# Optimization experiments

Measured on AMD Instinct MI355X. Metric: run time of the kernel, lower is better.

Reference implementation:

```python
import jax, jax.numpy as jnp
import numpy as np

N = 8192      # number of tree nodes
H = 256       # lstm_hiddens
D = 300       # word_dims (in_dim)
V = 50000     # vocab (n_embed)
K = 4         # max children per node (4-ary tree)
OUT = 4       # category_num


def _make_tree():
    # Static 4-ary tree: node i's children are 4i+1..4i+4 (if < N).
    idx = np.arange(N)[:, None] * K + 1 + np.arange(K)[None, :]
    mask = (idx < N).astype(np.float32)
    idx = np.where(idx < N, idx, 0)
    return jnp.asarray(idx, dtype=jnp.int32), jnp.asarray(mask, dtype=jnp.float32)


def setup_inputs() -> dict:
    key = jax.random.key(0)
    ks = jax.random.split(key, 6)
    xs = jax.random.randint(ks[0], (N,), 0, V, dtype=jnp.int32)
    emb_table = jax.random.normal(ks[1], (V, D), jnp.float32) * 0.1
    Wx = jax.random.normal(ks[2], (4, H, D), jnp.float32) * (1.0 / np.sqrt(D))
    bx = jnp.zeros((4, H), jnp.float32)
    Wh = jax.random.normal(ks[3], (4, H, H), jnp.float32) * (1.0 / np.sqrt(H))
    bh = jnp.zeros((4, H), jnp.float32)
    Wout = jax.random.normal(ks[4], (OUT, H), jnp.float32) * (1.0 / np.sqrt(H))
    bout = jnp.zeros((OUT,), jnp.float32)
    child_idx, child_mask = _make_tree()
    return dict(xs=xs, child_idx=child_idx, child_mask=child_mask,
                emb_table=emb_table, Wx=Wx, bx=bx, Wh=Wh, bh=bh,
                Wout=Wout, bout=bout)


def reference(xs, child_idx, child_mask, emb_table, Wx, bx, Wh, bh, Wout, bout):
    # Embedding lookup (dropout is identity in eval)
    X = emb_table[xs]                                   # [N, D]
    # Precompute all x-side gate projections in one batched matmul.
    # Gate order: 0=i, 1=f, 2=o, 3=u  (matches ix/fx/ox/ux).
    gx = jnp.einsum('ghd,nd->ngh', Wx, X) + bx          # [N, 4, H]

    Wh_i, Wh_f, Wh_o, Wh_u = Wh[0], Wh[1], Wh[2], Wh[3]
    bh_i, bh_f, bh_o, bh_u = bh[0], bh[1], bh[2], bh[3]

    def step(carry, i):
        Hbuf, Cbuf = carry
        cidx = child_idx[i]                              # [K]
        m = child_mask[i][:, None]                       # [K, 1]
        Hc = Hbuf[cidx] * m                              # [K, H] masked child h
        Cc = Cbuf[cidx] * m                              # [K, H] masked child c
        hs = Hc.sum(0)                                   # child_h_sum
        g = gx[i]                                        # [4, H]
        ig = jax.nn.sigmoid(g[0] + Wh_i @ hs + bh_i)
        og = jax.nn.sigmoid(g[2] + Wh_o @ hs + bh_o)
        ug = jnp.tanh(g[3] + Wh_u @ hs + bh_u)
        f = jax.nn.sigmoid(g[1] + Hc @ Wh_f.T + bh_f)    # [K, H] per-child forget
        c = ig * ug + (f * Cc).sum(0)                    # masked children have Cc=0
        h = og * jnp.tanh(c)
        return (Hbuf.at[i].set(h), Cbuf.at[i].set(c)), None

    order = jnp.arange(N - 1, -1, -1)                    # children before parents
    init = (jnp.zeros((N, H), X.dtype), jnp.zeros((N, H), X.dtype))
    (Hbuf, _), _ = jax.lax.scan(step, init, order)

    logits = Wout @ Hbuf[0] + bout                       # root output
    return jax.nn.log_softmax(logits)
```

## Files before the change

### kernel.cpp

```cpp
#include <hip/hip_runtime.h>


#define N_NODES 8192
#define HDIM 256
#define DDIM 300
#define GXC 1024
#define LEAF_FIRST 2048
#define WH_STRIDE 65536
#define XI(k) ((k) + (((k) >> 6) << 2))

__device__ __forceinline__ float sigf(float x) { return 1.0f / (1.0f + __expf(-x)); }

__global__ __launch_bounds__(256) void gx_gemm(
    const int* __restrict__ xs, const float* __restrict__ emb,
    const float* __restrict__ Wx, const float* __restrict__ bx,
    float* __restrict__ gx)
{
    const int lid  = blockIdx.x + blockIdx.y * gridDim.x;
    const int rowt = (lid & 7) * 8 + ((lid >> 3) & 7);
    const int colt = lid >> 6;
    const int n0 = rowt * 128;
    const int c0 = colt * 128;
    if (n0 >= LEAF_FIRST && (colt == 2 || colt == 3)) return;

    __shared__ __align__(16) float As[16][132];
    __shared__ __align__(16) float Bs[16][132];
    const int tid  = threadIdx.x;
    const int sr   = tid >> 1;
    const int sk8  = (tid & 1) << 3;
    const int trow = (tid >> 4) << 3;
    const int tcol = (tid & 15) << 3;

    const long arow = (long)xs[n0 + sr] * DDIM;
    const long brow = (long)(c0 + sr) * DDIM;

    float acc[8][8] = {};

    float4 a0 = *(const float4*)(emb + arow + sk8);
    float4 a1 = *(const float4*)(emb + arow + sk8 + 4);
    float4 b0 = *(const float4*)(Wx  + brow + sk8);
    float4 b1 = *(const float4*)(Wx  + brow + sk8 + 4);

    for (int k0 = 0; k0 < DDIM; k0 += 16) {
        __syncthreads();
        As[sk8+0][sr] = a0.x; As[sk8+1][sr] = a0.y; As[sk8+2][sr] = a0.z; As[sk8+3][sr] = a0.w;
        As[sk8+4][sr] = a1.x; As[sk8+5][sr] = a1.y; As[sk8+6][sr] = a1.z; As[sk8+7][sr] = a1.w;
        Bs[sk8+0][sr] = b0.x; Bs[sk8+1][sr] = b0.y; Bs[sk8+2][sr] = b0.z; Bs[sk8+3][sr] = b0.w;
        Bs[sk8+4][sr] = b1.x; Bs[sk8+5][sr] = b1.y; Bs[sk8+6][sr] = b1.z; Bs[sk8+7][sr] = b1.w;
        __syncthreads();

        const int kn = k0 + 16;
        a0 = make_float4(0.f,0.f,0.f,0.f); a1 = a0; b0 = a0; b1 = a0;
        if (kn < DDIM) {
            if (kn + sk8 < DDIM) {
                a0 = *(const float4*)(emb + arow + kn + sk8);
                b0 = *(const float4*)(Wx  + brow + kn + sk8);
            }
            if (kn + sk8 + 4 < DDIM) {
                a1 = *(const float4*)(emb + arow + kn + sk8 + 4);
                b1 = *(const float4*)(Wx  + brow + kn + sk8 + 4);
            }
        }

        #pragma unroll
        for (int k = 0; k < 16; k++) {
            const float4 av0 = *(const float4*)&As[k][trow];
            const float4 av1 = *(const float4*)&As[k][trow + 4];
            const float4 bv0 = *(const float4*)&Bs[k][tcol];
            const float4 bv1 = *(const float4*)&Bs[k][tcol + 4];
            const float aa[8] = {av0.x,av0.y,av0.z,av0.w,av1.x,av1.y,av1.z,av1.w};
            const float bb[8] = {bv0.x,bv0.y,bv0.z,bv0.w,bv1.x,bv1.y,bv1.z,bv1.w};
            #pragma unroll
            for (int i = 0; i < 8; i++)
                #pragma unroll
                for (int j = 0; j < 8; j++)
                    acc[i][j] = fmaf(aa[i], bb[j], acc[i][j]);
        }
    }

    const int col = c0 + tcol;
    const float4 bxa = *(const float4*)(bx + col);
    const float4 bxb = *(const float4*)(bx + col + 4);
    #pragma unroll
    for (int i = 0; i < 8; i++) {
        float4 r0, r1;
        r0.x = acc[i][0] + bxa.x; r0.y = acc[i][1] + bxa.y;
        r0.z = acc[i][2] + bxa.z; r0.w = acc[i][3] + bxa.w;
        r1.x = acc[i][4] + bxb.x; r1.y = acc[i][5] + bxb.y;
        r1.z = acc[i][6] + bxb.z; r1.w = acc[i][7] + bxb.w;
        float* dst = gx + (long)(n0 + trow + i) * GXC + col;
        *(float4*)dst = r0;
        *(float4*)(dst + 4) = r1;
    }
}

__global__ __launch_bounds__(256) void leaf_kernel(
    const float* __restrict__ gx, const float* __restrict__ bh,
    float* __restrict__ Hb, float* __restrict__ Cb)
{
    const int t = threadIdx.x;
    const float bi = bh[t], bo = bh[512 + t], bu = bh[768 + t];
    #pragma unroll
    for (int s = 0; s < 4; s++) {
        const int node = LEAF_FIRST + blockIdx.x * 4 + s;
        const float* g = gx + (long)node * GXC;
        const float gi = g[t]       + bi;
        const float go = g[512 + t] + bo;
        const float gu = g[768 + t] + bu;
        const float c  = sigf(gi) * tanhf(gu);
        const float h  = sigf(go) * tanhf(c);
        Hb[(long)node * HDIM + t] = h;
        Cb[(long)node * HDIM + t] = c;
    }
}

__global__ __launch_bounds__(256) void level_gemm(
    int first, int M, const float* __restrict__ Hb,
    const int* __restrict__ child_idx, const float* __restrict__ child_mask,
    const float* __restrict__ Wh, float* __restrict__ D)
{
    __shared__ __align__(16) float Xs[16][68];
    __shared__ __align__(16) float Ws[16][68];
    const int tid  = threadIdx.x;
    const int sec  = blockIdx.y;
    const int c0   = blockIdx.x * 64;
    const int r0   = blockIdx.z * 64;
    const int sr   = tid >> 2;
    const int sk   = (tid & 3) << 2;
    const int trow = (tid >> 4) << 2;
    const int tcol = (tid & 15) << 2;

    const float* Wg;
    if      (sec == 0) Wg = Wh;
    else if (sec == 1) Wg = Wh + 2 * WH_STRIDE;
    else if (sec == 2) Wg = Wh + 3 * WH_STRIDE;
    else               Wg = Wh + 1 * WH_STRIDE;

    const int  nl    = c0 + sr;
    const bool valid = nl < M;
    int   ci[4];
    float cm[4] = {0.f, 0.f, 0.f, 0.f};
    if (valid) {
        const int n = first + nl;
        if (sec < 3) {
            #pragma unroll
            for (int k = 0; k < 4; k++) {
                ci[k] = child_idx[n * 4 + k];
                cm[k] = child_mask[n * 4 + k];
            }
        } else {
            ci[0] = child_idx[n * 4 + (sec - 3)];
            cm[0] = child_mask[n * 4 + (sec - 3)];
        }
    }
    const long wrow = (long)(r0 + sr) * HDIM;

    float acc[4][4] = {};
    float4 hvr[4], wvr;

    #pragma unroll
    for (int k = 0; k < 4; k++) hvr[k] = make_float4(0.f, 0.f, 0.f, 0.f);
    if (valid) {
        if (sec < 3) {
            #pragma unroll
            for (int k = 0; k < 4; k++)
                if (cm[k] != 0.f)
                    hvr[k] = *(const float4*)(Hb + ci[k] * HDIM + sk);
        } else if (cm[0] != 0.f) {
            hvr[0] = *(const float4*)(Hb + ci[0] * HDIM + sk);
        }
    }
    wvr = *(const float4*)(Wg + wrow + sk);

    for (int k0 = 0; k0 < HDIM; k0 += 16) {
        __syncthreads();
        float4 xv;
        xv.x = hvr[0].x + hvr[1].x + hvr[2].x + hvr[3].x;
        xv.y = hvr[0].y + hvr[1].y + hvr[2].y + hvr[3].y;
        xv.z = hvr[0].z + hvr[1].z + hvr[2].z + hvr[3].z;
        xv.w = hvr[0].w + hvr[1].w + hvr[2].w + hvr[3].w;
        Xs[sk+0][sr] = xv.x; Xs[sk+1][sr] = xv.y; Xs[sk+2][sr] = xv.z; Xs[sk+3][sr] = xv.w;
        Ws[sk+0][sr] = wvr.x; Ws[sk+1][sr] = wvr.y; Ws[sk+2][sr] = wvr.z; Ws[sk+3][sr] = wvr.w;
        __syncthreads();

        const int kn = k0 + 16;
        if (kn < HDIM) {
            #pragma unroll
            for (int k = 0; k < 4; k++) hvr[k] = make_float4(0.f, 0.f, 0.f, 0.f);
            if (valid) {
                if (sec < 3) {
                    #pragma unroll
                    for (int k = 0; k < 4; k++)
                        if (cm[k] != 0.f)
                            hvr[k] = *(const float4*)(Hb + ci[k] * HDIM + kn + sk);
                } else if (cm[0] != 0.f) {
                    hvr[0] = *(const float4*)(Hb + ci[0] * HDIM + kn + sk);
                }
            }
            wvr = *(const float4*)(Wg + wrow + kn + sk);
        }

        #pragma unroll
        for (int k = 0; k < 16; k++) {
            float4 a = *(const float4*)&Ws[k][trow];
            float4 b = *(const float4*)&Xs[k][tcol];
            float avv[4] = {a.x, a.y, a.z, a.w};
            float bvv[4] = {b.x, b.y, b.z, b.w};
            #pragma unroll
            for (int i = 0; i < 4; i++)
                #pragma unroll
                for (int j = 0; j < 4; j++)
                    acc[i][j] = fmaf(avv[i], bvv[j], acc[i][j]);
        }
    }

    #pragma unroll
    for (int j = 0; j < 4; j++) {
        const int col = c0 + tcol + j;
        if (col < M) {
            float4 r;
            r.x = acc[0][j]; r.y = acc[1][j]; r.z = acc[2][j]; r.w = acc[3][j];
            *(float4*)(D + ((long)(sec * M + col)) * HDIM + r0 + trow) = r;
        }
    }
}

__global__ __launch_bounds__(256) void level_pointwise(
    int first, int M, int do_out,
    const float* __restrict__ gx, const float* __restrict__ D,
    const int* __restrict__ child_idx, const float* __restrict__ child_mask,
    const float* __restrict__ bh, float* __restrict__ Hb, float* __restrict__ Cb,
    const float* __restrict__ Wout, const float* __restrict__ bout,
    float* __restrict__ out)
{
    __shared__ float hroot[HDIM];
    __shared__ float logits[4];
    const int nl = blockIdx.x;
    const int n  = first + nl;
    const int t  = threadIdx.x;
    const float di  = D[((long)(0 * M + nl)) * HDIM + t];
    const float dO  = D[((long)(1 * M + nl)) * HDIM + t];
    const float du  = D[((long)(2 * M + nl)) * HDIM + t];
    const float* g = gx + (long)n * GXC;
    const float gi  = g[t]       + bh[t]       + di;
    const float gfb = g[256 + t] + bh[256 + t];
    const float go  = g[512 + t] + bh[512 + t] + dO;
    const float gu  = g[768 + t] + bh[768 + t] + du;

    float c = sigf(gi) * tanhf(gu);
    #pragma unroll
    for (int k = 0; k < 4; k++) {
        const float m = child_mask[n * 4 + k];
        if (m != 0.f) {
            const float df = D[((long)((3 + k) * M + nl)) * HDIM + t];
            const float cc = Cb[(long)child_idx[n * 4 + k] * HDIM + t];
            c = fmaf(sigf(gfb + df), cc, c);
        }
    }
    const float h = sigf(go) * tanhf(c);
    Hb[(long)n * HDIM + t] = h;
    Cb[(long)n * HDIM + t] = c;

    if (do_out) {
        hroot[t] = h;
        __syncthreads();
        const int o    = t >> 6;
        const int lane = t & 63;
        float s = 0.f;
        for (int jj = lane; jj < HDIM; jj += 64)
            s = fmaf(Wout[o * HDIM + jj], hroot[jj], s);
        #pragma unroll
        for (int off = 32; off > 0; off >>= 1)
            s += __shfl_down(s, off, 64);
        if (lane == 0) logits[o] = s + bout[o];
        __syncthreads();
        if (t == 0) {
            float m = logits[0];
            #pragma unroll
            for (int i = 1; i < 4; i++) m = fmaxf(m, logits[i]);
            float se = 0.f;
            #pragma unroll
            for (int i = 0; i < 4; i++) se += __expf(logits[i] - m);
            const float lse = m + __logf(se);
            #pragma unroll
            for (int i = 0; i < 4; i++) out[i] = logits[i] - lse;
        }
    }
}

__global__ __launch_bounds__(256) void tail_fused(
    int first, int M,
    const float* __restrict__ gx, const int* __restrict__ child_idx,
    const float* __restrict__ child_mask, const float* __restrict__ Wh,
    const float* __restrict__ bh, float* __restrict__ Hb, float* __restrict__ Cb)
{
    __shared__ __align__(16) float Xc[4][272];
    __shared__ __align__(16) float Xh[272];
    __shared__ float Ds[7][64];

    const int t  = threadIdx.x;
    const int nl = blockIdx.x;
    const int rb = blockIdx.y;
    const int n  = first + nl;

    {
        const int ch = t >> 6;
        const int e4 = (t & 63) << 2;
        const int cidx = child_idx[n * 4 + ch];
        const float m  = child_mask[n * 4 + ch];
        float4 v = make_float4(0.f, 0.f, 0.f, 0.f);
        if (m != 0.f) v = *(const float4*)(Hb + (long)cidx * HDIM + e4);
        *(float4*)&Xc[ch][XI(e4)] = v;
    }
    __syncthreads();
    {
        const int k = t;
        Xh[XI(k)] = Xc[0][XI(k)] + Xc[1][XI(k)] + Xc[2][XI(k)] + Xc[3][XI(k)];
    }
    __syncthreads();

    const int q = t >> 2, j = t & 3;
    const int row = rb * 64 + q;
    const float* Wi = Wh + 0 * WH_STRIDE + (long)row * HDIM;
    const float* Wf = Wh + 1 * WH_STRIDE + (long)row * HDIM;
    const float* Wo = Wh + 2 * WH_STRIDE + (long)row * HDIM;
    const float* Wu = Wh + 3 * WH_STRIDE + (long)row * HDIM;

    float a[7] = {};
    #pragma unroll 4
    for (int kk = j * 64; kk < j * 64 + 64; kk += 4) {
        const float4 wi = *(const float4*)(Wi + kk);
        const float4 wo = *(const float4*)(Wo + kk);
        const float4 wu = *(const float4*)(Wu + kk);
        const float4 wf = *(const float4*)(Wf + kk);
        const float4 hs = *(const float4*)&Xh[XI(kk)];
        a[0] += wi.x*hs.x + wi.y*hs.y + wi.z*hs.z + wi.w*hs.w;
        a[1] += wo.x*hs.x + wo.y*hs.y + wo.z*hs.z + wo.w*hs.w;
        a[2] += wu.x*hs.x + wu.y*hs.y + wu.z*hs.z + wu.w*hs.w;
        #pragma unroll
        for (int ch = 0; ch < 4; ch++) {
            const float4 cv = *(const float4*)&Xc[ch][XI(kk)];
            a[3 + ch] += wf.x*cv.x + wf.y*cv.y + wf.z*cv.z + wf.w*cv.w;
        }
    }
    #pragma unroll
    for (int s = 0; s < 7; s++) {
        float v = a[s];
        v += __shfl_xor(v, 1, 64);
        v += __shfl_xor(v, 2, 64);
        if (j == 0) Ds[s][q] = v;
    }
    __syncthreads();

    if (t < 64) {
        const int r = rb * 64 + t;
        const float* g = gx + (long)n * GXC;
        const float gi  = g[r]       + bh[r]       + Ds[0][t];
        const float gfb = g[256 + r] + bh[256 + r];
        const float go  = g[512 + r] + bh[512 + r] + Ds[1][t];
        const float gu  = g[768 + r] + bh[768 + r] + Ds[2][t];
        float c = sigf(gi) * tanhf(gu);
        #pragma unroll
        for (int ch = 0; ch < 4; ch++) {
            const float m = child_mask[n * 4 + ch];
            if (m != 0.f) {
                const float cc = Cb[(long)child_idx[n * 4 + ch] * HDIM + r];
                c = fmaf(sigf(gfb + Ds[3 + ch][t]), cc, c);
            }
        }
        const float h = sigf(go) * tanhf(c);
        Hb[(long)n * HDIM + r] = h;
        Cb[(long)n * HDIM + r] = c;
    }
}

extern "C" void kernel_launch(void* const* d_in, const int* in_sizes, int n_in,
                              void* d_out, int out_size, void* d_ws, size_t ws_size,
                              hipStream_t stream)
{
    const int*   xs         = (const int*)  d_in[0];
    const int*   child_idx  = (const int*)  d_in[1];
    const float* child_mask = (const float*)d_in[2];
    const float* emb        = (const float*)d_in[3];
    const float* Wx         = (const float*)d_in[4];
    const float* bx         = (const float*)d_in[5];
    const float* Wh         = (const float*)d_in[6];
    const float* bh         = (const float*)d_in[7];
    const float* Wout       = (const float*)d_in[8];
    const float* bout       = (const float*)d_in[9];
    float* out = (float*)d_out;

    float* gxb = (float*)d_ws;
    float* Hb  = gxb + (size_t)N_NODES * GXC;
    float* Cb  = Hb  + (size_t)N_NODES * HDIM;
    float* Dbuf = gxb + (size_t)LEAF_FIRST * GXC;

    gx_gemm<<<dim3(8, 64), 256, 0, stream>>>(xs, emb, Wx, bx, gxb);
    leaf_kernel<<<(N_NODES - LEAF_FIRST) / 4, 256, 0, stream>>>(gxb, bh, Hb, Cb);

    const int pfb[3] = {1365, 341, 85};
    const int pcb[3] = { 683, 1024, 256};
    for (int p = 0; p < 3; p++) {
        const int M = pcb[p];
        dim3 grid((M + 63) / 64, 7, 4);
        level_gemm<<<grid, 256, 0, stream>>>(pfb[p], M, Hb, child_idx, child_mask,
                                             Wh, Dbuf);
        level_pointwise<<<M, 256, 0, stream>>>(pfb[p], M, 0, gxb, Dbuf, child_idx,
                                               child_mask, bh, Hb, Cb,
                                               Wout, bout, out);
    }

    const int pft[3] = {21, 5, 1};
    const int pct[3] = {64, 16, 4};
    for (int p = 0; p < 3; p++) {
        dim3 grid(pct[p], 4);
        tail_fused<<<grid, 256, 0, stream>>>(pft[p], pct[p], gxb, child_idx,
                                             child_mask, Wh, bh, Hb, Cb);
    }

    {
        dim3 grid(1, 7, 4);
        level_gemm<<<grid, 256, 0, stream>>>(0, 1, Hb, child_idx, child_mask,
                                             Wh, Dbuf);
        level_pointwise<<<1, 256, 0, stream>>>(0, 1, 1, gxb, Dbuf, child_idx,
                                               child_mask, bh, Hb, Cb,
                                               Wout, bout, out);
    }
}
```

Measured before the change: 307.8 us.

## Fuse root level into single kernel, move level-85 to tail path, fix GEMM LDS layout

The root node's two launches (level_gemm plus level_pointwise with the output head) become one root_kernel that does the Wh matvecs, the cell update and the log-softmax in a single block. The 256-node level moves from the two-kernel GEMM path to the fused tail kernel, saving two launches. The gx GEMM thread mapping changes from contiguous 8-wide slabs to two 4-wide slabs 64 apart, which is meant to cut LDS bank conflicts on the shared-memory reads. The root kernel runs the whole Wh matvec on one block, serialising that work, and the fused tail kernel may parallelise a 256-node level less well than the GEMM path.

```diff
diff --git a/kernel.cpp b/kernel.cpp
--- a/kernel.cpp
+++ b/kernel.cpp
@@ -25,11 +25,11 @@
 
     __shared__ __align__(16) float As[16][132];
     __shared__ __align__(16) float Bs[16][132];
-    const int tid  = threadIdx.x;
-    const int sr   = tid >> 1;
-    const int sk8  = (tid & 1) << 3;
-    const int trow = (tid >> 4) << 3;
-    const int tcol = (tid & 15) << 3;
+    const int tid   = threadIdx.x;
+    const int sr    = tid >> 1;
+    const int sk8   = (tid & 1) << 3;
+    const int trow4 = (tid >> 4) << 2;
+    const int tcol4 = (tid & 15) << 2;
 
     const long arow = (long)xs[n0 + sr] * DDIM;
     const long brow = (long)(c0 + sr) * DDIM;
@@ -64,10 +64,10 @@
 
         #pragma unroll
         for (int k = 0; k < 16; k++) {
-            const float4 av0 = *(const float4*)&As[k][trow];
-            const float4 av1 = *(const float4*)&As[k][trow + 4];
-            const float4 bv0 = *(const float4*)&Bs[k][tcol];
-            const float4 bv1 = *(const float4*)&Bs[k][tcol + 4];
+            const float4 av0 = *(const float4*)&As[k][trow4];
+            const float4 av1 = *(const float4*)&As[k][64 + trow4];
+            const float4 bv0 = *(const float4*)&Bs[k][tcol4];
+            const float4 bv1 = *(const float4*)&Bs[k][64 + tcol4];
             const float aa[8] = {av0.x,av0.y,av0.z,av0.w,av1.x,av1.y,av1.z,av1.w};
             const float bb[8] = {bv0.x,bv0.y,bv0.z,bv0.w,bv1.x,bv1.y,bv1.z,bv1.w};
             #pragma unroll
@@ -78,19 +78,19 @@
         }
     }
 
-    const int col = c0 + tcol;
-    const float4 bxa = *(const float4*)(bx + col);
-    const float4 bxb = *(const float4*)(bx + col + 4);
+    const float4 bxa = *(const float4*)(bx + c0 + tcol4);
+    const float4 bxb = *(const float4*)(bx + c0 + 64 + tcol4);
     #pragma unroll
     for (int i = 0; i < 8; i++) {
+        const int row = n0 + ((i < 4) ? (trow4 + i) : (64 + trow4 + i - 4));
         float4 r0, r1;
         r0.x = acc[i][0] + bxa.x; r0.y = acc[i][1] + bxa.y;
         r0.z = acc[i][2] + bxa.z; r0.w = acc[i][3] + bxa.w;
         r1.x = acc[i][4] + bxb.x; r1.y = acc[i][5] + bxb.y;
         r1.z = acc[i][6] + bxb.z; r1.w = acc[i][7] + bxb.w;
-        float* dst = gx + (long)(n0 + trow + i) * GXC + col;
-        *(float4*)dst = r0;
-        *(float4*)(dst + 4) = r1;
+        float* dst = gx + (long)row * GXC + c0;
+        *(float4*)(dst + tcol4)      = r0;
+        *(float4*)(dst + 64 + tcol4) = r1;
     }
 }
 
@@ -226,15 +226,10 @@
 }
 
 __global__ __launch_bounds__(256) void level_pointwise(
-    int first, int M, int do_out,
-    const float* __restrict__ gx, const float* __restrict__ D,
+    int first, int M, const float* __restrict__ gx, const float* __restrict__ D,
     const int* __restrict__ child_idx, const float* __restrict__ child_mask,
-    const float* __restrict__ bh, float* __restrict__ Hb, float* __restrict__ Cb,
-    const float* __restrict__ Wout, const float* __restrict__ bout,
-    float* __restrict__ out)
-{
-    __shared__ float hroot[HDIM];
-    __shared__ float logits[4];
+    const float* __restrict__ bh, float* __restrict__ Hb, float* __restrict__ Cb)
+{
     const int nl = blockIdx.x;
     const int n  = first + nl;
     const int t  = threadIdx.x;
@@ -260,32 +255,6 @@
     const float h = sigf(go) * tanhf(c);
     Hb[(long)n * HDIM + t] = h;
     Cb[(long)n * HDIM + t] = c;
-
-    if (do_out) {
-        hroot[t] = h;
-        __syncthreads();
-        const int o    = t >> 6;
-        const int lane = t & 63;
-        float s = 0.f;
-        for (int jj = lane; jj < HDIM; jj += 64)
-            s = fmaf(Wout[o * HDIM + jj], hroot[jj], s);
-        #pragma unroll
-        for (int off = 32; off > 0; off >>= 1)
-            s += __shfl_down(s, off, 64);
-        if (lane == 0) logits[o] = s + bout[o];
-        __syncthreads();
-        if (t == 0) {
-            float m = logits[0];
-            #pragma unroll
-            for (int i = 1; i < 4; i++) m = fmaxf(m, logits[i]);
-            float se = 0.f;
-            #pragma unroll
-            for (int i = 0; i < 4; i++) se += __expf(logits[i] - m);
-            const float lse = m + __logf(se);
-            #pragma unroll
-            for (int i = 0; i < 4; i++) out[i] = logits[i] - lse;
-        }
-    }
 }
 
 __global__ __launch_bounds__(256) void tail_fused(
@@ -374,6 +343,102 @@
     }
 }
 
+__global__ __launch_bounds__(256) void root_kernel(
+    const float* __restrict__ gx, const int* __restrict__ child_idx,
+    const float* __restrict__ child_mask, const float* __restrict__ Wh,
+    const float* __restrict__ bh, float* __restrict__ Hb, float* __restrict__ Cb,
+    const float* __restrict__ Wout, const float* __restrict__ bout,
+    float* __restrict__ out)
+{
+    __shared__ __align__(16) float Xc[4][272];
+    __shared__ __align__(16) float Xh[272];
+    __shared__ float hroot[HDIM];
+    __shared__ float logits[4];
+
+    const int t = threadIdx.x;
+
+    {
+        const int ch = t >> 6;
+        const int e4 = (t & 63) << 2;
+        const int cidx = child_idx[ch];
+        const float m  = child_mask[ch];
+        float4 v = make_float4(0.f, 0.f, 0.f, 0.f);
+        if (m != 0.f) v = *(const float4*)(Hb + (long)cidx * HDIM + e4);
+        *(float4*)&Xc[ch][XI(e4)] = v;
+    }
+    __syncthreads();
+    Xh[XI(t)] = Xc[0][XI(t)] + Xc[1][XI(t)] + Xc[2][XI(t)] + Xc[3][XI(t)];
+    __syncthreads();
+
+    const float* Wi = Wh + 0 * WH_STRIDE + (long)t * HDIM;
+    const float* Wf = Wh + 1 * WH_STRIDE + (long)t * HDIM;
+    const float* Wo = Wh + 2 * WH_STRIDE + (long)t * HDIM;
+    const float* Wu = Wh + 3 * WH_STRIDE + (long)t * HDIM;
+    float a[7] = {};
+    #pragma unroll 4
+    for (int kk = 0; kk < HDIM; kk += 4) {
+        const float4 wi = *(const float4*)(Wi + kk);
+        const float4 wo = *(const float4*)(Wo + kk);
+        const float4 wu = *(const float4*)(Wu + kk);
+        const float4 wf = *(const float4*)(Wf + kk);
+        const float4 hs = *(const float4*)&Xh[XI(kk)];
+        a[0] += wi.x*hs.x + wi.y*hs.y + wi.z*hs.z + wi.w*hs.w;
+        a[1] += wo.x*hs.x + wo.y*hs.y + wo.z*hs.z + wo.w*hs.w;
+        a[2] += wu.x*hs.x + wu.y*hs.y + wu.z*hs.z + wu.w*hs.w;
+        #pragma unroll
+        for (int ch = 0; ch < 4; ch++) {
+            const float4 cv = *(const float4*)&Xc[ch][XI(kk)];
+            a[3 + ch] += wf.x*cv.x + wf.y*cv.y + wf.z*cv.z + wf.w*cv.w;
+        }
+    }
+
+    {
+        const float* g = gx;
+        const float gi  = g[t]       + bh[t]       + a[0];
+        const float gfb = g[256 + t] + bh[256 + t];
+        const float go  = g[512 + t] + bh[512 + t] + a[1];
+        const float gu  = g[768 + t] + bh[768 + t] + a[2];
+        float c = sigf(gi) * tanhf(gu);
+        #pragma unroll
+        for (int ch = 0; ch < 4; ch++) {
+            const float m = child_mask[ch];
+            if (m != 0.f) {
+                const float cc = Cb[(long)child_idx[ch] * HDIM + t];
+                c = fmaf(sigf(gfb + a[3 + ch]), cc, c);
+            }
+        }
+        const float h = sigf(go) * tanhf(c);
+        Hb[t] = h;
+        Cb[t] = c;
+        hroot[t] = h;
+    }
+    __syncthreads();
+
+    {
+        const int o    = t >> 6;
+        const int lane = t & 63;
+        float s = 0.f;
+        for (int jj = lane; jj < HDIM; jj += 64)
+            s = fmaf(Wout[o * HDIM + jj], hroot[jj], s);
+        #pragma unroll
+        for (int off = 32; off > 0; off >>= 1)
+            s += __shfl_down(s, off, 64);
+        if (lane == 0) logits[o] = s + bout[o];
+        __syncthreads();
+        if (t == 0) {
+            float m = logits[0];
+            #pragma unroll
+            for (int i = 1; i < 4; i++) m = fmaxf(m, logits[i]);
+            float se = 0.f;
+            #pragma unroll
+            for (int i = 0; i < 4; i++) se += __expf(logits[i] - m);
+            const float lse = m + __logf(se);
+            #pragma unroll
+            for (int i = 0; i < 4; i++) out[i] = logits[i] - lse;
+        }
+    }
+}
+
 extern "C" void kernel_launch(void* const* d_in, const int* in_sizes, int n_in,
                               void* d_out, int out_size, void* d_ws, size_t ws_size,
                               hipStream_t stream)
@@ -398,32 +463,25 @@
     gx_gemm<<<dim3(8, 64), 256, 0, stream>>>(xs, emb, Wx, bx, gxb);
     leaf_kernel<<<(N_NODES - LEAF_FIRST) / 4, 256, 0, stream>>>(gxb, bh, Hb, Cb);
 
-    const int pfb[3] = {1365, 341, 85};
-    const int pcb[3] = { 683, 1024, 256};
-    for (int p = 0; p < 3; p++) {
+    const int pfb[2] = {1365, 341};
+    const int pcb[2] = { 683, 1024};
+    for (int p = 0; p < 2; p++) {
         const int M = pcb[p];
         dim3 grid((M + 63) / 64, 7, 4);
         level_gemm<<<grid, 256, 0, stream>>>(pfb[p], M, Hb, child_idx, child_mask,
                                              Wh, Dbuf);
-        level_pointwise<<<M, 256, 0, stream>>>(pfb[p], M, 0, gxb, Dbuf, child_idx,
-                                               child_mask, bh, Hb, Cb,
-                                               Wout, bout, out);
-    }
-
-    const int pft[3] = {21, 5, 1};
-    const int pct[3] = {64, 16, 4};
-    for (int p = 0; p < 3; p++) {
+        level_pointwise<<<M, 256, 0, stream>>>(pfb[p], M, gxb, Dbuf, child_idx,
+                                               child_mask, bh, Hb, Cb);
+    }
+
+    const int pft[4] = {85, 21, 5, 1};
+    const int pct[4] = {256, 64, 16, 4};
+    for (int p = 0; p < 4; p++) {
         dim3 grid(pct[p], 4);
         tail_fused<<<grid, 256, 0, stream>>>(pft[p], pct[p], gxb, child_idx,
                                              child_mask, Wh, bh, Hb, Cb);
     }
 
-    {
-        dim3 grid(1, 7, 4);
-        level_gemm<<<grid, 256, 0, stream>>>(0, 1, Hb, child_idx, child_mask,
-                                             Wh, Dbuf);
-        level_pointwise<<<1, 256, 0, stream>>>(0, 1, 1, gxb, Dbuf, child_idx,
-                                               child_mask, bh, Hb, Cb,
-                                               Wout, bout, out);
-    }
-}
+    root_kernel<<<1, 256, 0, stream>>>(gxb, child_idx, child_mask, Wh, bh,
+                                       Hb, Cb, Wout, bout, out);
+}
```

Measured after the change: 326.9 us. 6.2% more time.
